# Optimization experiments

Hardware: AMD Instinct MI355X
Metric: run time of the kernel (lower is better)

## Reference

```python
import jax, jax.numpy as jnp
import numpy as np
from jax import lax

CONV_SIZE = 5
MORPH_SIZE = 5
TH1_INIT = 0.5
STEP = 0.0005
LO, HI = 0.84, 0.86


def _maxpool(a):
    p = MORPH_SIZE // 2
    return lax.reduce_window(
        a, -jnp.inf, lax.max,
        window_dimensions=(1, 1, MORPH_SIZE, MORPH_SIZE),
        window_strides=(1, 1, 1, 1),
        padding=[(0, 0), (0, 0), (p, p), (p, p)])


def setup_inputs() -> dict:
    key = jax.random.key(0)
    k1, _ = jax.random.split(key)
    x = jax.random.uniform(k1, (8, 4, 1024, 1024), dtype=jnp.float32)
    blur_k = jnp.full((1, 1, CONV_SIZE, CONV_SIZE), 1.0 / CONV_SIZE ** 2, dtype=jnp.float32)
    return {"x": x, "blur_k": blur_k}


def reference(x, blur_k):
    N, c, h, w = x.shape
    xi = x.reshape(N * c, 1, h, w)
    out = lax.conv_general_dilated(
        xi, blur_k, window_strides=(1, 1), padding='SAME',
        dimension_numbers=('NCHW', 'OIHW', 'NCHW')).reshape(N, c, h, w)

    # iterative mean-based threshold (quantile) search, same as the torch while-loops
    out_c = lax.stop_gradient(out)

    def frac_above(th):
        return jnp.mean(jnp.where(out_c > th, 1.0, 0.0))

    th = jnp.float32(TH1_INIT)
    th = lax.while_loop(lambda t: frac_above(t) < LO, lambda t: t - STEP, th)
    th = lax.while_loop(lambda t: frac_above(t) > HI, lambda t: t + STEP, th)

    thr = jnp.where(out > th, 1.0, 0.0)
    # morphological close: max-pool then min-pool (min = -maxpool(-x))
    closed = -_maxpool(-_maxpool(thr))
    return closed  # torch casts to float64; kept float32 (see notes)
```

## Files before the change

### kernel.cpp

```cpp
#include <hip/hip_runtime.h>


#define K_STEPS 1024
#define LO_COUNT 28185723u
#define R_TILE 16
#define PT_ROWS 16

#define OFF_HIST 4096
#define OFF_KQ   16384

struct TTable { float v[K_STEPS]; };
static constexpr TTable make_T() {
    TTable t{};
    float th = 0.5f;
    for (int k = 0; k < K_STEPS; k++) { t.v[k] = th; th = th - 0.0005f; }
    return t;
}
__device__ constexpr TTable Tc = make_T();

__device__ __forceinline__ uint4 cvt4(float4 f) {
    return make_uint4((unsigned int)(f.x * 8388608.0f),
                      (unsigned int)(f.y * 8388608.0f),
                      (unsigned int)(f.z * 8388608.0f),
                      (unsigned int)(f.w * 8388608.0f));
}

__device__ __forceinline__ int find_ki(const unsigned int* __restrict__ Us,
                                       float U0f, unsigned int s) {
    float g = (U0f - (float)s) * 9.5367432e-6f;
    int lo = (int)g;
    lo = max(0, min(1021, lo));
    unsigned int a0 = Us[lo], a1 = Us[lo + 1], a2 = Us[lo + 2];
    return lo + (int)(s < a0) + (int)(s < a1) + (int)(s < a2);
}

__global__ __launch_bounds__(256, 4) void
k_pass1(const float4* __restrict__ x4, const float* __restrict__ bk,
        unsigned int* __restrict__ hist, unsigned short* __restrict__ kq16) {
    __shared__ unsigned int Us[K_STEPS];
    __shared__ unsigned int lh[K_STEPS + 1];
    int tid = threadIdx.x;
    int p = blockIdx.y, y0 = blockIdx.x * R_TILE;

    {
        double c = (double)bk[0] * (1.0 / 8388608.0);
        #pragma unroll
        for (int i = 0; i < 4; i++) {
            int k = tid + 256 * i;
            double T = (double)Tc.v[k];
            unsigned int u = 0u;
            if (T >= 0.0) {
                u = (unsigned int)(floor(T / c) + 1.0);
                while (u > 0u && (double)(u - 1u) * c > T) u--;
                while (!((double)u * c > T)) u++;
            }
            Us[k] = u;
        }
    }
    for (int i = tid; i < K_STEPS + 1; i += 256) lh[i] = 0u;
    __syncthreads();
    float U0f = (float)Us[0];

    const float4* pf = x4 + (size_t)p * 262144;
    int tB = (tid < 255) ? tid + 1 : 0;
    const uint4 z4 = make_uint4(0u, 0u, 0u, 0u);

    unsigned int cs0 = 0, cs1 = 0, cs2 = 0, cs3 = 0,
                 cs4 = 0, cs5 = 0, cs6 = 0, cs7 = 0;
    {
        float4 ra[5], rb[5];
        #pragma unroll
        for (int i = 0; i < 5; i++) {
            int yy = y0 - 2 + i, yc = min(max(yy, 0), 1023);
            ra[i] = pf[yc * 256 + tid];
            rb[i] = pf[yc * 256 + tB];
        }
        #pragma unroll
        for (int i = 0; i < 5; i++) {
            bool v = (unsigned)(y0 - 2 + i) < 1024u;
            uint4 a = v ? cvt4(ra[i]) : z4;
            uint4 b = v ? cvt4(rb[i]) : z4;
            cs0 += a.x; cs1 += a.y; cs2 += a.z; cs3 += a.w;
            cs4 += b.x; cs5 += b.y; cs6 += b.z; cs7 += b.w;
        }
    }
    float4 N0a, N0b, N1a, N1b, O0a, O0b, O1a, O1b;
    {
        int yn0 = min(y0 + 3, 1023), yn1 = min(y0 + 4, 1023);
        int yo0 = max(y0 - 2, 0),    yo1 = max(y0 - 1, 0);
        N0a = pf[yn0 * 256 + tid]; N0b = pf[yn0 * 256 + tB];
        N1a = pf[yn1 * 256 + tid]; N1b = pf[yn1 * 256 + tB];
        O0a = pf[yo0 * 256 + tid]; O0b = pf[yo0 * 256 + tB];
        O1a = pf[yo1 * 256 + tid]; O1b = pf[yo1 * 256 + tB];
    }

    unsigned int cnt0 = 0;
    int wlane = tid & 63;
    #pragma unroll 4
    for (int iy = 0; iy < R_TILE; iy++) {
        int y = y0 + iy;

        unsigned int m123 = cs1 + cs2 + cs3;
        unsigned int h45  = cs4 + cs5;
        unsigned int v0, v1, v2, v3;
        if (tid != 255) {
            v0 = cs0 + m123 + cs4;
            v1 = m123 + h45;
            v2 = cs2 + cs3 + h45 + cs6;
            v3 = cs3 + h45 + cs6 + cs7;
        } else {
            v0 = cs0 + m123;
            v1 = m123;
            v2 = h45 + cs6;
            v3 = h45 + cs6 + cs7;
        }

        int k0 = find_ki(Us, U0f, v0);
        int k1 = find_ki(Us, U0f, v1);
        int k2 = find_ki(Us, U0f, v2);
        int k3 = find_ki(Us, U0f, v3);
        cnt0 += (unsigned)(k0 == 0) + (unsigned)(k1 == 0)
              + (unsigned)(k2 == 0) + (unsigned)(k3 == 0);
        if (k0 > 0) atomicAdd(&lh[k0], 1u);
        if (k1 > 0) atomicAdd(&lh[k1], 1u);
        if (k2 > 0) atomicAdd(&lh[k2], 1u);
        if (k3 > 0) atomicAdd(&lh[k3], 1u);

        unsigned int pa = (unsigned)min(k0, 255) | ((unsigned)min(k1, 255) << 8);
        unsigned int pb = (unsigned)min(k2, 255) | ((unsigned)min(k3, 255) << 8);
        unsigned int paN = __shfl_down(pa, 1);
        size_t rb = ((size_t)p * 1024 + (size_t)y) * 512;
        if (wlane < 63) {
            ((unsigned int*)(kq16 + rb))[tid + 1] = pb | (paN << 16);
        } else {
            kq16[rb + ((tid < 255) ? (unsigned)(2 * tid + 2) : 0u)] =
                (unsigned short)pb;
        }
        if (wlane == 0) kq16[rb + 2 * tid + 1] = (unsigned short)pa;

        {
            bool vn = (unsigned)(y + 3) < 1024u;
            bool vo = (y - 2) >= 0;
            uint4 na = vn ? cvt4(N0a) : z4;
            uint4 nb = vn ? cvt4(N0b) : z4;
            uint4 oa = vo ? cvt4(O0a) : z4;
            uint4 ob = vo ? cvt4(O0b) : z4;
            cs0 += na.x - oa.x; cs1 += na.y - oa.y;
            cs2 += na.z - oa.z; cs3 += na.w - oa.w;
            cs4 += nb.x - ob.x; cs5 += nb.y - ob.y;
            cs6 += nb.z - ob.z; cs7 += nb.w - ob.w;
        }
        N0a = N1a; N0b = N1b; O0a = O1a; O0b = O1b;
        {
            int yn = min(y + 5, 1023);
            N1a = pf[yn * 256 + tid]; N1b = pf[yn * 256 + tB];
            O1a = pf[y * 256 + tid];  O1b = pf[y * 256 + tB];
        }
    }

    #pragma unroll
    for (int d = 32; d > 0; d >>= 1) cnt0 += __shfl_down(cnt0, d);
    if ((tid & 63) == 0 && cnt0) atomicAdd(&lh[0], cnt0);
    __syncthreads();
    for (int i = tid; i < K_STEPS + 1; i += 256) {
        unsigned int c = lh[i];
        if (c) atomicAdd(&hist[i], c);
    }
}

__global__ __launch_bounds__(256) void
k_post(const unsigned char* __restrict__ kqb, const unsigned int* __restrict__ hist,
       float* __restrict__ out) {
    __shared__ unsigned long long Tt[24 * 16];
    __shared__ unsigned long long Vv[20 * 16];
    __shared__ unsigned long long Dd[20 * 16];
    __shared__ unsigned long long Ww[16 * 16];
    __shared__ unsigned long long Ff[16 * 16];
    __shared__ int ksS;

    int tid = threadIdx.x;
    int p = blockIdx.y, y0 = blockIdx.x * PT_ROWS;

    if (tid < 64) {
        int lane = tid;
        unsigned int h[16], s = 0;
        #pragma unroll
        for (int i = 0; i < 16; i++) { h[i] = hist[lane * 16 + i]; s += h[i]; }
        unsigned int inc = s;
        #pragma unroll
        for (int d = 1; d < 64; d <<= 1) {
            unsigned int t = __shfl_up(inc, d);
            if (lane >= d) inc += t;
        }
        unsigned int excl = inc - s;
        bool cross = (excl < LO_COUNT) && (excl + s >= LO_COUNT);
        unsigned long long m = __ballot(cross);
        if (m) {
            int cl = __ffsll((long long)m) - 1;
            if (lane == cl) {
                unsigned int c = excl; int ks = K_STEPS - 1;
                for (int i = 0; i < 16; i++) { c += h[i]; if (c >= LO_COUNT) { ks = lane * 16 + i; break; } }
                ksS = ks;
            }
        } else if (lane == 0) ksS = K_STEPS - 1;
    }
    __syncthreads();
    int ks = ksS;

    const unsigned char* kp = kqb + (size_t)p * 1048576;
    unsigned short* Tt16 = (unsigned short*)Tt;
    #pragma unroll
    for (int i = 0; i < 6; i++) {
        int ch = tid + 256 * i;
        int r = ch >> 6, cc = ch & 63;
        int pr = y0 - 4 + r;
        unsigned int m = 0u;
        if ((unsigned)pr < 1024u) {
            uint4 q = ((const uint4*)(kp + (size_t)pr * 1024))[cc];
            unsigned int wv;
            wv = q.x;
            m |= (unsigned)((wv & 0xffu) <= (unsigned)ks)
               | ((unsigned)(((wv >> 8) & 0xffu) <= (unsigned)ks) << 1)
               | ((unsigned)(((wv >> 16) & 0xffu) <= (unsigned)ks) << 2)
               | ((unsigned)((wv >> 24) <= (unsigned)ks) << 3);
            wv = q.y;
            m |= ((unsigned)((wv & 0xffu) <= (unsigned)ks) << 4)
               | ((unsigned)(((wv >> 8) & 0xffu) <= (unsigned)ks) << 5)
               | ((unsigned)(((wv >> 16) & 0xffu) <= (unsigned)ks) << 6)
               | ((unsigned)((wv >> 24) <= (unsigned)ks) << 7);
            wv = q.z;
            m |= ((unsigned)((wv & 0xffu) <= (unsigned)ks) << 8)
               | ((unsigned)(((wv >> 8) & 0xffu) <= (unsigned)ks) << 9)
               | ((unsigned)(((wv >> 16) & 0xffu) <= (unsigned)ks) << 10)
               | ((unsigned)((wv >> 24) <= (unsigned)ks) << 11);
            wv = q.w;
            m |= ((unsigned)((wv & 0xffu) <= (unsigned)ks) << 12)
               | ((unsigned)(((wv >> 8) & 0xffu) <= (unsigned)ks) << 13)
               | ((unsigned)(((wv >> 16) & 0xffu) <= (unsigned)ks) << 14)
               | ((unsigned)((wv >> 24) <= (unsigned)ks) << 15);
        }
        Tt16[ch] = (unsigned short)m;
    }
    __syncthreads();

    for (int i = tid; i < 320; i += 256) {
        int vr = i >> 4, wc = i & 15;
        int b = vr * 16 + wc;
        Vv[i] = Tt[b] | Tt[b + 16] | Tt[b + 32] | Tt[b + 48] | Tt[b + 64];
    }
    __syncthreads();

    for (int i = tid; i < 320; i += 256) {
        int vr = i >> 4, wc = i & 15;
        int pr = y0 - 2 + vr;
        if ((unsigned)pr >= 1024u) { Dd[i] = ~0ull; continue; }
        unsigned long long Vc = Vv[i];
        unsigned long long Vl = (wc > 0)  ? Vv[i - 1] : 0ull;
        unsigned long long Vr = (wc < 15) ? Vv[i + 1] : 0ull;
        Dd[i] = Vc
            | (Vc << 1) | (Vl >> 63)
            | (Vc << 2) | (Vl >> 62)
            | (Vc >> 1) | (Vr << 63)
            | (Vc >> 2) | (Vr << 62);
    }
    __syncthreads();

    {
        int wr = tid >> 4, wc = tid & 15;
        int b = wr * 16 + wc;
        Ww[tid] = Dd[b] & Dd[b + 16] & Dd[b + 32] & Dd[b + 48] & Dd[b + 64];
    }
    __syncthreads();

    {
        int wc = tid & 15;
        unsigned long long Wc = Ww[tid];
        unsigned long long Wl = (wc > 0)  ? Ww[tid - 1] : ~0ull;
        unsigned long long Wr = (wc < 15) ? Ww[tid + 1] : ~0ull;
        Ff[tid] = Wc
            & ((Wc << 1) | (Wl >> 63))
            & ((Wc << 2) | (Wl >> 62))
            & ((Wc >> 1) | (Wr << 63))
            & ((Wc >> 2) | (Wr << 62));
    }
    __syncthreads();

    for (int i = 0; i < PT_ROWS; i++) {
        unsigned long long wd = Ff[i * 16 + (tid >> 4)];
        int sh = (tid & 15) * 4;
        float4 f;
        f.x = (float)((wd >> sh) & 1ull);
        f.y = (float)((wd >> (sh + 1)) & 1ull);
        f.z = (float)((wd >> (sh + 2)) & 1ull);
        f.w = (float)((wd >> (sh + 3)) & 1ull);
        ((float4*)(out + (size_t)p * 1048576 + (size_t)(y0 + i) * 1024))[tid] = f;
    }
}

extern "C" void kernel_launch(void* const* d_in, const int* in_sizes, int n_in,
                              void* d_out, int out_size, void* d_ws, size_t ws_size,
                              hipStream_t stream) {
    const float4* x4 = (const float4*)d_in[0];
    const float*  bk = (const float*)d_in[1];
    float* out = (float*)d_out;

    char* ws = (char*)d_ws;
    unsigned int*   hist = (unsigned int*)(ws + OFF_HIST);
    unsigned short* kq16 = (unsigned short*)(ws + OFF_KQ);
    const unsigned char* kqb = (const unsigned char*)(ws + OFF_KQ);

    hipMemsetAsync(hist, 0, (K_STEPS + 1) * sizeof(unsigned int), stream);

    dim3 g1(1024 / R_TILE, 32);
    k_pass1<<<g1, 256, 0, stream>>>(x4, bk, hist, kq16);

    dim3 g2(1024 / PT_ROWS, 32);
    k_post<<<g2, 256, 0, stream>>>(kqb, hist, out);
}
```

Baseline: 282.2 us.

## Share neighbor column sums via shuffles, trim search, raise occupancy, nontemporal stores

Pass1 no longer loads and converts the neighbouring float4 for every thread. It takes the right neighbour's column sums through a wave shuffle, and only the last lane of each wave keeps loading its neighbour. This halves global loads and roughly halves the conversion and accumulation work. The threshold lookup now uses an FMA with a precomputed bias and two comparisons instead of three. Launch bounds rise to 8 blocks per CU, and the post kernel writes its output with nontemporal stores. The two-compare lookup assumes the rounded estimate is within one step of the true index, and the higher occupancy target may cause register spills.

```diff
diff --git a/kernel.cpp b/kernel.cpp
--- a/kernel.cpp
+++ b/kernel.cpp
@@ -8,6 +8,8 @@
 
 #define OFF_HIST 4096
 #define OFF_KQ   16384
+
+typedef float  fx4 __attribute__((ext_vector_type(4)));
 
 struct TTable { float v[K_STEPS]; };
 static constexpr TTable make_T() {
@@ -26,21 +28,22 @@
 }
 
 __device__ __forceinline__ int find_ki(const unsigned int* __restrict__ Us,
-                                       float U0f, unsigned int s) {
-    float g = (U0f - (float)s) * 9.5367432e-6f;
+                                       float gbias, unsigned int s) {
+    float g = fmaf(-(float)s, 9.5367432e-6f, gbias);
     int lo = (int)g;
-    lo = max(0, min(1021, lo));
-    unsigned int a0 = Us[lo], a1 = Us[lo + 1], a2 = Us[lo + 2];
-    return lo + (int)(s < a0) + (int)(s < a1) + (int)(s < a2);
-}
-
-__global__ __launch_bounds__(256, 4) void
+    lo = max(0, min(1022, lo));
+    unsigned int a0 = Us[lo], a1 = Us[lo + 1];
+    return lo + (int)(s < a0) + (int)(s < a1);
+}
+
+__global__ __launch_bounds__(256, 8) void
 k_pass1(const float4* __restrict__ x4, const float* __restrict__ bk,
         unsigned int* __restrict__ hist, unsigned short* __restrict__ kq16) {
     __shared__ unsigned int Us[K_STEPS];
     __shared__ unsigned int lh[K_STEPS + 1];
     int tid = threadIdx.x;
     int p = blockIdx.y, y0 = blockIdx.x * R_TILE;
+    int wlane = tid & 63;
 
     {
         double c = (double)bk[0] * (1.0 / 8388608.0);
@@ -59,66 +62,73 @@
     }
     for (int i = tid; i < K_STEPS + 1; i += 256) lh[i] = 0u;
     __syncthreads();
-    float U0f = (float)Us[0];
+    float gbias = fmaf((float)Us[0], 9.5367432e-6f, 0.5f);
 
     const float4* pf = x4 + (size_t)p * 262144;
     int tB = (tid < 255) ? tid + 1 : 0;
     const uint4 z4 = make_uint4(0u, 0u, 0u, 0u);
-
-    unsigned int cs0 = 0, cs1 = 0, cs2 = 0, cs3 = 0,
-                 cs4 = 0, cs5 = 0, cs6 = 0, cs7 = 0;
+    bool edge = (wlane == 63);
+
+    unsigned int cs0 = 0, cs1 = 0, cs2 = 0, cs3 = 0;
+    unsigned int cb0 = 0, cb1 = 0, cb2 = 0, cb3 = 0;
     {
         float4 ra[5], rb[5];
         #pragma unroll
         for (int i = 0; i < 5; i++) {
             int yy = y0 - 2 + i, yc = min(max(yy, 0), 1023);
             ra[i] = pf[yc * 256 + tid];
-            rb[i] = pf[yc * 256 + tB];
+            if (edge) rb[i] = pf[yc * 256 + tB];
         }
         #pragma unroll
         for (int i = 0; i < 5; i++) {
             bool v = (unsigned)(y0 - 2 + i) < 1024u;
             uint4 a = v ? cvt4(ra[i]) : z4;
-            uint4 b = v ? cvt4(rb[i]) : z4;
             cs0 += a.x; cs1 += a.y; cs2 += a.z; cs3 += a.w;
-            cs4 += b.x; cs5 += b.y; cs6 += b.z; cs7 += b.w;
-        }
-    }
-    float4 N0a, N0b, N1a, N1b, O0a, O0b, O1a, O1b;
+            if (edge) {
+                uint4 b = v ? cvt4(rb[i]) : z4;
+                cb0 += b.x; cb1 += b.y; cb2 += b.z; cb3 += b.w;
+            }
+        }
+    }
+    float4 N0a, N1a, O0a, O1a, NBa, OBa;
     {
         int yn0 = min(y0 + 3, 1023), yn1 = min(y0 + 4, 1023);
         int yo0 = max(y0 - 2, 0),    yo1 = max(y0 - 1, 0);
-        N0a = pf[yn0 * 256 + tid]; N0b = pf[yn0 * 256 + tB];
-        N1a = pf[yn1 * 256 + tid]; N1b = pf[yn1 * 256 + tB];
-        O0a = pf[yo0 * 256 + tid]; O0b = pf[yo0 * 256 + tB];
-        O1a = pf[yo1 * 256 + tid]; O1b = pf[yo1 * 256 + tB];
+        N0a = pf[yn0 * 256 + tid]; N1a = pf[yn1 * 256 + tid];
+        O0a = pf[yo0 * 256 + tid]; O1a = pf[yo1 * 256 + tid];
+        if (edge) { NBa = pf[yn0 * 256 + tB]; OBa = pf[yo0 * 256 + tB]; }
     }
 
     unsigned int cnt0 = 0;
-    int wlane = tid & 63;
     #pragma unroll 4
     for (int iy = 0; iy < R_TILE; iy++) {
         int y = y0 + iy;
 
+        unsigned int nc0 = __shfl_down(cs0, 1);
+        unsigned int nc1 = __shfl_down(cs1, 1);
+        unsigned int nc2 = __shfl_down(cs2, 1);
+        unsigned int nc3 = __shfl_down(cs3, 1);
+        if (edge) { nc0 = cb0; nc1 = cb1; nc2 = cb2; nc3 = cb3; }
+
         unsigned int m123 = cs1 + cs2 + cs3;
-        unsigned int h45  = cs4 + cs5;
+        unsigned int h45  = nc0 + nc1;
         unsigned int v0, v1, v2, v3;
         if (tid != 255) {
-            v0 = cs0 + m123 + cs4;
+            v0 = cs0 + m123 + nc0;
             v1 = m123 + h45;
-            v2 = cs2 + cs3 + h45 + cs6;
-            v3 = cs3 + h45 + cs6 + cs7;
+            v2 = cs2 + cs3 + h45 + nc2;
+            v3 = cs3 + h45 + nc2 + nc3;
         } else {
             v0 = cs0 + m123;
             v1 = m123;
-            v2 = h45 + cs6;
-            v3 = h45 + cs6 + cs7;
-        }
-
-        int k0 = find_ki(Us, U0f, v0);
-        int k1 = find_ki(Us, U0f, v1);
-        int k2 = find_ki(Us, U0f, v2);
-        int k3 = find_ki(Us, U0f, v3);
+            v2 = h45 + nc2;
+            v3 = h45 + nc2 + nc3;
+        }
+
+        int k0 = find_ki(Us, gbias, v0);
+        int k1 = find_ki(Us, gbias, v1);
+        int k2 = find_ki(Us, gbias, v2);
+        int k3 = find_ki(Us, gbias, v3);
         cnt0 += (unsigned)(k0 == 0) + (unsigned)(k1 == 0)
               + (unsigned)(k2 == 0) + (unsigned)(k3 == 0);
         if (k0 > 0) atomicAdd(&lh[k0], 1u);
@@ -142,19 +152,26 @@
             bool vn = (unsigned)(y + 3) < 1024u;
             bool vo = (y - 2) >= 0;
             uint4 na = vn ? cvt4(N0a) : z4;
-            uint4 nb = vn ? cvt4(N0b) : z4;
             uint4 oa = vo ? cvt4(O0a) : z4;
-            uint4 ob = vo ? cvt4(O0b) : z4;
             cs0 += na.x - oa.x; cs1 += na.y - oa.y;
             cs2 += na.z - oa.z; cs3 += na.w - oa.w;
-            cs4 += nb.x - ob.x; cs5 += nb.y - ob.y;
-            cs6 += nb.z - ob.z; cs7 += nb.w - ob.w;
-        }
-        N0a = N1a; N0b = N1b; O0a = O1a; O0b = O1b;
+            if (edge) {
+                uint4 nb = vn ? cvt4(NBa) : z4;
+                uint4 ob = vo ? cvt4(OBa) : z4;
+                cb0 += nb.x - ob.x; cb1 += nb.y - ob.y;
+                cb2 += nb.z - ob.z; cb3 += nb.w - ob.w;
+            }
+        }
+        N0a = N1a; O0a = O1a;
         {
             int yn = min(y + 5, 1023);
-            N1a = pf[yn * 256 + tid]; N1b = pf[yn * 256 + tB];
-            O1a = pf[y * 256 + tid];  O1b = pf[y * 256 + tB];
+            N1a = pf[yn * 256 + tid];
+            O1a = pf[y * 256 + tid];
+            if (edge) {
+                int ynb = min(y + 4, 1023), yob = max(y - 1, 0);
+                NBa = pf[ynb * 256 + tB];
+                OBa = pf[yob * 256 + tB];
+            }
         }
     }
 
@@ -288,12 +305,13 @@
     for (int i = 0; i < PT_ROWS; i++) {
         unsigned long long wd = Ff[i * 16 + (tid >> 4)];
         int sh = (tid & 15) * 4;
-        float4 f;
+        fx4 f;
         f.x = (float)((wd >> sh) & 1ull);
         f.y = (float)((wd >> (sh + 1)) & 1ull);
         f.z = (float)((wd >> (sh + 2)) & 1ull);
         f.w = (float)((wd >> (sh + 3)) & 1ull);
-        ((float4*)(out + (size_t)p * 1048576 + (size_t)(y0 + i) * 1024))[tid] = f;
+        fx4* dst = (fx4*)(out + (size_t)p * 1048576 + (size_t)(y0 + i) * 1024) + tid;
+        __builtin_nontemporal_store(f, dst);
     }
 }
 
@@ -309,7 +327,7 @@
     unsigned short* kq16 = (unsigned short*)(ws + OFF_KQ);
     const unsigned char* kqb = (const unsigned char*)(ws + OFF_KQ);
 
-    hipMemsetAsync(hist, 0, (K_STEPS + 1) * sizeof(unsigned int), stream);
+    (void)hipMemsetAsync(hist, 0, (K_STEPS + 1) * sizeof(unsigned int), stream);
 
     dim3 g1(1024 / R_TILE, 32);
     k_pass1<<<g1, 256, 0, stream>>>(x4, bk, hist, kq16);
```

Result: slower. 292.8 us (+3.8%).
